# Kernel optimization log

Hardware: AMD Instinct MI355X
Metric: run time of the kernel (lower is better)

The kernel has to match this reference:

```python
import jax, jax.numpy as jnp
import numpy as np

N, E, IN_C, HID, OUT_C, HEADS, NUM_CLASSES = 50000, 800000, 128, 64, 64, 4, 40
NEG_SLOPE = 0.2


def _gat_conv(x, src, dst, W, a_src, a_dst, bias, heads, concat):
    # x: [N, F_in]; W: [F_in, heads*C]; a_src/a_dst: [1, heads, C]; bias: [out]
    n = x.shape[0]
    h = (x @ W).reshape(n, heads, -1)                      # [N, H, C]
    alpha_s = (h * a_src).sum(-1)                          # [N, H]
    alpha_d = (h * a_dst).sum(-1)                          # [N, H]
    e = jax.nn.leaky_relu(alpha_s[src] + alpha_d[dst], NEG_SLOPE)  # [E, H]
    # scatter-softmax over incoming edges of each dst node
    emax = jax.ops.segment_max(e, dst, num_segments=n)
    emax = jnp.where(jnp.isfinite(emax), emax, 0.0)
    ee = jnp.exp(e - emax[dst])
    denom = jax.ops.segment_sum(ee, dst, num_segments=n) + 1e-16
    w = ee / denom[dst]                                    # [E, H]
    out = jax.ops.segment_sum(h[src] * w[:, :, None], dst, num_segments=n)  # [N, H, C]
    out = out.reshape(n, -1) if concat else out.mean(axis=1)
    return out + bias


def setup_inputs() -> dict:
    key = jax.random.key(0)
    ks = jax.random.split(key, 12)
    s1 = 1.0 / np.sqrt(IN_C)
    s2 = 1.0 / np.sqrt(HID * HEADS)
    s3 = 1.0 / np.sqrt(OUT_C)
    return {
        "x": jax.random.normal(ks[0], (N, IN_C), dtype=jnp.float32),
        "edge_index": jax.random.randint(ks[1], (2, E), 0, N, dtype=jnp.int64),
        "W1": jax.random.normal(ks[2], (IN_C, HEADS * HID), dtype=jnp.float32) * s1,
        "att_src1": jax.random.normal(ks[3], (1, HEADS, HID), dtype=jnp.float32) * s1,
        "att_dst1": jax.random.normal(ks[4], (1, HEADS, HID), dtype=jnp.float32) * s1,
        "b1": jnp.zeros((HEADS * HID,), dtype=jnp.float32),
        "W2": jax.random.normal(ks[5], (HEADS * HID, OUT_C), dtype=jnp.float32) * s2,
        "att_src2": jax.random.normal(ks[6], (1, 1, OUT_C), dtype=jnp.float32) * s2,
        "att_dst2": jax.random.normal(ks[7], (1, 1, OUT_C), dtype=jnp.float32) * s2,
        "b2": jnp.zeros((OUT_C,), dtype=jnp.float32),
        "fc_w": jax.random.normal(ks[8], (OUT_C, NUM_CLASSES), dtype=jnp.float32) * s3,
        "fc_b": jnp.zeros((NUM_CLASSES,), dtype=jnp.float32),
    }


def reference(x, edge_index, W1, att_src1, att_dst1, b1, W2, att_src2, att_dst2, b2, fc_w, fc_b):
    n = x.shape[0]
    loops = jnp.arange(n, dtype=edge_index.dtype)
    ei = jnp.concatenate([edge_index, jnp.stack([loops, loops])], axis=1)  # add self-loops (PyG default)
    src, dst = ei[0], ei[1]
    h = jax.nn.relu(_gat_conv(x, src, dst, W1, att_src1, att_dst1, b1, HEADS, True))
    h = jax.nn.relu(_gat_conv(h, src, dst, W2, att_src2, att_dst2, b2, 1, False))
    # dropout p=0.01 is identity in eval mode
    pooled = h.mean(axis=0, keepdims=True)                 # global mean pool -> [1, OUT_C]
    logits = pooled @ fc_w + fc_b
    return jax.nn.log_softmax(logits, axis=1)
```

## Files before the change

kernel.cpp:

```cpp
#include <hip/hip_runtime.h>
#include <hip/hip_bf16.h>
#include <math.h>

#define NEG_SLOPE 0.2f
#define CHUNK2 2048
#define PGROUPS 32

typedef __attribute__((ext_vector_type(8))) short bf16x8;
typedef __attribute__((ext_vector_type(4))) float f32x4;
typedef __attribute__((ext_vector_type(2))) float f32x2_t;

__device__ __forceinline__ float lrelu(float a) { return a >= 0.f ? a : NEG_SLOPE * a; }
__device__ __forceinline__ unsigned short f2bu(float v) {
  unsigned u = __float_as_uint(v);
  u += 0x7fffu + ((u >> 16) & 1u);
  return (unsigned short)(u >> 16);
}
__device__ __forceinline__ unsigned char f2fp8(float v) {
  return (unsigned char)(__builtin_amdgcn_cvt_pk_fp8_f32(v, v, 0, false) & 0xFF);
}

__global__ __launch_bounds__(256) void prep_kernel(
    const float* __restrict__ W1, unsigned short* __restrict__ w1t,
    const float* __restrict__ W2, unsigned short* __restrict__ w2t,
    const int* __restrict__ ei, int* __restrict__ bhist,
    int E0, int Etot, int NBUCK, int wBlocks, int histBlocks) {
  __shared__ int hsm[256];
  int t = threadIdx.x;
  if (blockIdx.x < (unsigned)wBlocks) {
    const int tot1 = 128 * 256, tot2 = 256 * 64;
    for (int i = blockIdx.x * 256 + t; i < tot1 + tot2; i += wBlocks * 256) {
      if (i < tot1) { int k = i >> 8, n = i & 255; w1t[n * 128 + k] = f2bu(W1[i]); }
      else { int j = i - tot1; int k = j >> 6, n = j & 63; w2t[n * 256 + k] = f2bu(W2[j]); }
    }
  } else {
    int bid = blockIdx.x - wBlocks;
    hsm[t] = 0;
    __syncthreads();
    for (int e = bid * 256 + t; e < Etot; e += histBlocks * 256) {
      int dst = (e < E0) ? ei[E0 + e] : (e - E0);
      atomicAdd(&hsm[dst >> 8], 1);
    }
    __syncthreads();
    if (t < NBUCK && hsm[t]) atomicAdd(&bhist[t], hsm[t]);
  }
}

__global__ __launch_bounds__(256) void bucket_scan_kernel(const int* __restrict__ bhist,
    int* __restrict__ bucketOff, int* __restrict__ cursor, int* __restrict__ rowptrN,
    float* __restrict__ pooled_grp, int NBUCK, int Etot) {
  __shared__ int s[256];
  int t = threadIdx.x;
  int v = (t < NBUCK) ? bhist[t] : 0;
  s[t] = v;
  __syncthreads();
  for (int off = 1; off < 256; off <<= 1) {
    int u = (t >= off) ? s[t - off] : 0;
    __syncthreads();
    s[t] += u;
    __syncthreads();
  }
  int excl = s[t] - v;
  if (t < NBUCK) { bucketOff[t] = excl; cursor[t] = excl; }
  if (t == 0) { bucketOff[NBUCK] = Etot; *rowptrN = Etot; }
  for (int i = t; i < PGROUPS * 64; i += 256) pooled_grp[i] = 0.f;
}

__device__ void gemm1_tile(const float* __restrict__ x,
    const unsigned short* __restrict__ BT, unsigned char* __restrict__ C8,
    const float* __restrict__ att_s, const float* __restrict__ att_d,
    float* __restrict__ as_, float* __restrict__ ad_,
    int M, int bx, int by, char* smem) {
  const int K = 128;
  unsigned short (*Al)[40] = (unsigned short (*)[40])smem;
  unsigned short (*Bt)[40] = (unsigned short (*)[40])(smem + 5120);
  float* sal = (float*)(smem + 10240);
  float* sad = (float*)(smem + 10752);
  const int tid = threadIdx.x;
  const int row0 = by * 64, col0 = bx * 64;
  const int lane = tid & 63, wave = tid >> 6;
  const int wm = wave >> 1, wn = wave & 1;
  const int l15 = lane & 15, q = lane >> 4;

  f32x4 acc[2][2] = {};

  const int rr = tid >> 2, rc = (tid & 3) * 8;

  for (int k0 = 0; k0 < K; k0 += 32) {
    float4 v0 = make_float4(0.f, 0.f, 0.f, 0.f), v1 = v0;
    if (row0 + rr < M) {
      const float* ap = x + (size_t)(row0 + rr) * K + k0 + rc;
      v0 = *(const float4*)ap;
      v1 = *(const float4*)(ap + 4);
    }
    *(ushort4*)&Al[rr][rc] = make_ushort4(f2bu(v0.x), f2bu(v0.y), f2bu(v0.z), f2bu(v0.w));
    *(ushort4*)&Al[rr][rc + 4] = make_ushort4(f2bu(v1.x), f2bu(v1.y), f2bu(v1.z), f2bu(v1.w));
    {
      const ushort4* bp = (const ushort4*)(BT + (size_t)(col0 + rr) * K + k0 + rc);
      *(ushort4*)&Bt[rr][rc] = bp[0];
      *(ushort4*)&Bt[rr][rc + 4] = bp[1];
    }
    __syncthreads();
    bf16x8 af[2], bf[2];
#pragma unroll
    for (int mi = 0; mi < 2; mi++)
      af[mi] = *(const bf16x8*)&Al[wm * 32 + mi * 16 + l15][q * 8];
#pragma unroll
    for (int ni = 0; ni < 2; ni++)
      bf[ni] = *(const bf16x8*)&Bt[wn * 32 + ni * 16 + l15][q * 8];
#pragma unroll
    for (int mi = 0; mi < 2; mi++)
#pragma unroll
      for (int ni = 0; ni < 2; ni++)
        acc[mi][ni] = __builtin_amdgcn_mfma_f32_16x16x32_bf16(af[mi], bf[ni], acc[mi][ni], 0, 0, 0);
    __syncthreads();
  }
#pragma unroll
  for (int mi = 0; mi < 2; mi++) {
#pragma unroll
    for (int r = 0; r < 4; r++) {
      int grow = row0 + wm * 32 + mi * 16 + q * 4 + r;
      if (grow < M) {
#pragma unroll
        for (int ni = 0; ni < 2; ni++) {
          int gcol = col0 + wn * 32 + ni * 16 + l15;
          C8[(size_t)grow * 256 + gcol] = f2fp8(acc[mi][ni][r]);
        }
      }
    }
  }
  float atts0 = att_s[col0 + wn * 32 + l15];
  float atts1 = att_s[col0 + wn * 32 + 16 + l15];
  float attd0 = att_d[col0 + wn * 32 + l15];
  float attd1 = att_d[col0 + wn * 32 + 16 + l15];
#pragma unroll
  for (int mi = 0; mi < 2; mi++) {
#pragma unroll
    for (int r = 0; r < 4; r++) {
      float vs = acc[mi][0][r] * atts0 + acc[mi][1][r] * atts1;
      float vd = acc[mi][0][r] * attd0 + acc[mi][1][r] * attd1;
#pragma unroll
      for (int off = 1; off < 16; off <<= 1) {
        vs += __shfl_xor(vs, off);
        vd += __shfl_xor(vd, off);
      }
      if (l15 == 0) {
        int rl = wm * 32 + mi * 16 + q * 4 + r;
        sal[wn * 64 + rl] = vs;
        sad[wn * 64 + rl] = vd;
      }
    }
  }
  __syncthreads();
  if (tid < 64) {
    int grow = row0 + tid;
    if (grow < M) {
      as_[(size_t)grow * 4 + bx] = sal[tid] + sal[64 + tid];
      ad_[(size_t)grow * 4 + bx] = sad[tid] + sad[64 + tid];
    }
  }
}

__global__ __launch_bounds__(256) void gemm1_scatter_kernel(
    const float* __restrict__ x, const unsigned short* __restrict__ BT,
    unsigned char* __restrict__ C8, const float* __restrict__ att_s,
    const float* __restrict__ att_d, float* __restrict__ as_, float* __restrict__ ad_,
    int M, const int* __restrict__ ei, int* __restrict__ cursor, int* __restrict__ pairs,
    int E0, int Etot, int NBUCK, int NSC) {
  __shared__ __align__(16) char smem[18432];
  if (blockIdx.x < (unsigned)NSC) {
    int2* stage = (int2*)smem;
    int* h = (int*)(smem + 16384);
    int* base = (int*)(smem + 17408);
    int t = threadIdx.x;
    int e0 = blockIdx.x * CHUNK2;
    h[t] = 0;
    __syncthreads();
    int cnt = Etot - e0;
    if (cnt > CHUNK2) cnt = CHUNK2;
    for (int i = t; i < cnt; i += 256) {
      int e = e0 + i;
      int s, d;
      if (e < E0) { s = ei[e]; d = ei[E0 + e]; } else { s = d = e - E0; }
      stage[i] = make_int2((s << 8) | (d & 255), d >> 8);
      atomicAdd(&h[d >> 8], 1);
    }
    __syncthreads();
    if (t < NBUCK && h[t]) base[t] = atomicAdd(&cursor[t], h[t]);
    __syncthreads();
    for (int i = t; i < cnt; i += 256) {
      int2 p = stage[i];
      int pos = atomicAdd(&base[p.y], 1);
      pairs[pos] = p.x;
    }
  } else {
    int flat = blockIdx.x - NSC;
    gemm1_tile(x, BT, C8, att_s, att_d, as_, ad_, M, flat % 4, flat / 4, smem);
  }
}

__global__ __launch_bounds__(256) void csr_build_kernel(const int* __restrict__ pairs,
    const int* __restrict__ bucketOff, int* __restrict__ rowptr, int* __restrict__ csr_src,
    int N) {
  int b = blockIdx.x, t = threadIdx.x;
  int base = bucketOff[b], cnt = bucketOff[b + 1] - base;
  int n0 = b << 8;
  __shared__ int h[256];
  __shared__ int s[256];
  __shared__ int ex[256];
  h[t] = 0;
  __syncthreads();
  for (int i = t; i < cnt; i += 256) atomicAdd(&h[pairs[base + i] & 255], 1);
  __syncthreads();
  int v = h[t];
  s[t] = v;
  __syncthreads();
  for (int off = 1; off < 256; off <<= 1) {
    int u = (t >= off) ? s[t - off] : 0;
    __syncthreads();
    s[t] += u;
    __syncthreads();
  }
  ex[t] = s[t] - v;
  if (n0 + t < N) rowptr[n0 + t] = base + ex[t];
  __syncthreads();
  for (int i = t; i < cnt; i += 256) {
    int p = pairs[base + i];
    int pos = atomicAdd(&ex[p & 255], 1);
    csr_src[base + pos] = ((unsigned)p) >> 8;
  }
}

#define ACCV(W, X) do {                                                        \
    f32x2_t w2_; w2_.x = (W); w2_.y = (W);                                     \
    av[0] += w2_ * __builtin_amdgcn_cvt_pk_f32_fp8((X).x, false);              \
    av[1] += w2_ * __builtin_amdgcn_cvt_pk_f32_fp8((X).x, true);               \
    av[2] += w2_ * __builtin_amdgcn_cvt_pk_f32_fp8((X).y, false);              \
    av[3] += w2_ * __builtin_amdgcn_cvt_pk_f32_fp8((X).y, true);               \
    av[4] += w2_ * __builtin_amdgcn_cvt_pk_f32_fp8((X).z, false);              \
    av[5] += w2_ * __builtin_amdgcn_cvt_pk_f32_fp8((X).z, true);               \
    av[6] += w2_ * __builtin_amdgcn_cvt_pk_f32_fp8((X).w, false);              \
    av[7] += w2_ * __builtin_amdgcn_cvt_pk_f32_fp8((X).w, true);               \
  } while (0)

__global__ __launch_bounds__(256) void aggr1_kernel(const int* __restrict__ rowptr,
    const int* __restrict__ csr_src, const float* __restrict__ as_,
    const float* __restrict__ ad_, const uint4* __restrict__ h1f8,
    const float* __restrict__ b1, unsigned short* __restrict__ out1, int Nn) {
  int lane = threadIdx.x & 63, wv = threadIdx.x >> 6;
  int q = lane >> 4, l15 = lane & 15;
  int n = (blockIdx.x * 4 + wv) * 4 + q;
  if (n >= Nn) return;
  int row = rowptr[n], deg = rowptr[n + 1] - row;
  int rowEnd = row + deg;
  int hh = l15 >> 2;
  float adv = ad_[n * 4 + hh];
  const uint4* hb = h1f8 + l15;
  f32x2_t av[8] = {};
  float wsum = 0.f;
  int p0 = row + l15;
  int idxv = (p0 < rowEnd) ? csr_src[p0] : 0;
  for (int s0 = 0; s0 < deg; s0 += 16) {
    int pn = row + s0 + 16 + l15;
    int idxn = (pn < rowEnd) ? csr_src[pn] : 0;
    int m = deg - s0;
    if (m > 16) m = 16;
    int j = 0;
    for (; j + 4 <= m; j += 4) {
      int i0 = __shfl(idxv, j, 16);
      int i1 = __shfl(idxv, j + 1, 16);
      int i2 = __shfl(idxv, j + 2, 16);
      int i3 = __shfl(idxv, j + 3, 16);
      float a0v = as_[i0 * 4 + hh];
      float a1v = as_[i1 * 4 + hh];
      float a2v = as_[i2 * 4 + hh];
      float a3v = as_[i3 * 4 + hh];
      uint4 x0 = hb[(size_t)i0 * 16];
      uint4 x1 = hb[(size_t)i1 * 16];
      uint4 x2 = hb[(size_t)i2 * 16];
      uint4 x3 = hb[(size_t)i3 * 16];
      float w0 = __expf(lrelu(a0v + adv));
      float w1 = __expf(lrelu(a1v + adv));
      float w2 = __expf(lrelu(a2v + adv));
      float w3 = __expf(lrelu(a3v + adv));
      wsum += (w0 + w1) + (w2 + w3);
      ACCV(w0, x0);
      ACCV(w1, x1);
      ACCV(w2, x2);
      ACCV(w3, x3);
    }
    for (; j < m; j++) {
      int i0 = __shfl(idxv, j, 16);
      float a0v = as_[i0 * 4 + hh];
      uint4 x0 = hb[(size_t)i0 * 16];
      float w0 = __expf(lrelu(a0v + adv));
      wsum += w0;
      ACCV(w0, x0);
    }
    idxv = idxn;
  }
  float vinv = 1.f / wsum;
  int c0i = l15 * 16;
  unsigned short ob[16];
#pragma unroll
  for (int k = 0; k < 4; k++) {
    float4 bb = *(const float4*)(b1 + c0i + k * 4);
    float r0 = fmaf(av[k * 2].x, vinv, bb.x);
    float r1 = fmaf(av[k * 2].y, vinv, bb.y);
    float r2 = fmaf(av[k * 2 + 1].x, vinv, bb.z);
    float r3 = fmaf(av[k * 2 + 1].y, vinv, bb.w);
    ob[k * 4 + 0] = f2bu(r0 > 0.f ? r0 : 0.f);
    ob[k * 4 + 1] = f2bu(r1 > 0.f ? r1 : 0.f);
    ob[k * 4 + 2] = f2bu(r2 > 0.f ? r2 : 0.f);
    ob[k * 4 + 3] = f2bu(r3 > 0.f ? r3 : 0.f);
  }
  *(ushort4*)(out1 + (size_t)n * 256 + c0i) = *(ushort4*)&ob[0];
  *(ushort4*)(out1 + (size_t)n * 256 + c0i + 4) = *(ushort4*)&ob[4];
  *(ushort4*)(out1 + (size_t)n * 256 + c0i + 8) = *(ushort4*)&ob[8];
  *(ushort4*)(out1 + (size_t)n * 256 + c0i + 12) = *(ushort4*)&ob[12];
}

__global__ __launch_bounds__(256) void gemm2_kernel(const unsigned short* __restrict__ A,
    const unsigned short* __restrict__ BT, unsigned char* __restrict__ C8,
    const float* __restrict__ att_s, const float* __restrict__ att_d,
    float* __restrict__ as_, float* __restrict__ ad_, int M) {
  const int K = 256, Ncol = 64;
  __shared__ __align__(16) char smem[11264];
  unsigned short (*Al)[40] = (unsigned short (*)[40])smem;
  unsigned short (*Bt)[40] = (unsigned short (*)[40])(smem + 5120);
  float* sal = (float*)(smem + 10240);
  float* sad = (float*)(smem + 10752);
  const int tid = threadIdx.x;
  const int row0 = blockIdx.x * 64;
  const int lane = tid & 63, wave = tid >> 6;
  const int wm = wave >> 1, wn = wave & 1;
  const int l15 = lane & 15, q = lane >> 4;

  f32x4 acc[2][2] = {};
  const int rr = tid >> 2, rc = (tid & 3) * 8;

  for (int k0 = 0; k0 < K; k0 += 32) {
    ushort4 av0 = make_ushort4(0, 0, 0, 0), av1 = av0;
    if (row0 + rr < M) {
      const ushort4* ap = (const ushort4*)(A + (size_t)(row0 + rr) * K + k0 + rc);
      av0 = ap[0]; av1 = ap[1];
    }
    *(ushort4*)&Al[rr][rc] = av0;
    *(ushort4*)&Al[rr][rc + 4] = av1;
    {
      const ushort4* bp = (const ushort4*)(BT + (size_t)rr * K + k0 + rc);
      *(ushort4*)&Bt[rr][rc] = bp[0];
      *(ushort4*)&Bt[rr][rc + 4] = bp[1];
    }
    __syncthreads();
    bf16x8 af[2], bf[2];
#pragma unroll
    for (int mi = 0; mi < 2; mi++)
      af[mi] = *(const bf16x8*)&Al[wm * 32 + mi * 16 + l15][q * 8];
#pragma unroll
    for (int ni = 0; ni < 2; ni++)
      bf[ni] = *(const bf16x8*)&Bt[wn * 32 + ni * 16 + l15][q * 8];
#pragma unroll
    for (int mi = 0; mi < 2; mi++)
#pragma unroll
      for (int ni = 0; ni < 2; ni++)
        acc[mi][ni] = __builtin_amdgcn_mfma_f32_16x16x32_bf16(af[mi], bf[ni], acc[mi][ni], 0, 0, 0);
    __syncthreads();
  }
#pragma unroll
  for (int mi = 0; mi < 2; mi++) {
#pragma unroll
    for (int r = 0; r < 4; r++) {
      int grow = row0 + wm * 32 + mi * 16 + q * 4 + r;
      if (grow < M) {
#pragma unroll
        for (int ni = 0; ni < 2; ni++) {
          int gcol = wn * 32 + ni * 16 + l15;
          C8[(size_t)grow * Ncol + gcol] = f2fp8(acc[mi][ni][r]);
        }
      }
    }
  }
  float atts0 = att_s[wn * 32 + l15], atts1 = att_s[wn * 32 + 16 + l15];
  float attd0 = att_d[wn * 32 + l15], attd1 = att_d[wn * 32 + 16 + l15];
#pragma unroll
  for (int mi = 0; mi < 2; mi++) {
#pragma unroll
    for (int r = 0; r < 4; r++) {
      float vs = acc[mi][0][r] * atts0 + acc[mi][1][r] * atts1;
      float vd = acc[mi][0][r] * attd0 + acc[mi][1][r] * attd1;
#pragma unroll
      for (int off = 1; off < 16; off <<= 1) {
        vs += __shfl_xor(vs, off);
        vd += __shfl_xor(vd, off);
      }
      if (l15 == 0) {
        int rl = wm * 32 + mi * 16 + q * 4 + r;
        sal[wn * 64 + rl] = vs;
        sad[wn * 64 + rl] = vd;
      }
    }
  }
  __syncthreads();
  if (tid < 64) {
    int grow = row0 + tid;
    if (grow < M) {
      as_[grow] = sal[tid] + sal[64 + tid];
      ad_[grow] = sad[tid] + sad[64 + tid];
    }
  }
}

__global__ __launch_bounds__(256) void aggr2_pool_kernel(const int* __restrict__ rowptr,
    const int* __restrict__ csr_src, const float* __restrict__ as_,
    const float* __restrict__ ad_, const unsigned* __restrict__ h2f8,
    const float* __restrict__ b2, float* __restrict__ pooled_grp, int Nn) {
  int lane = threadIdx.x & 63, wv = threadIdx.x >> 6;
  int q = lane >> 4, l15 = lane & 15;
  int c0 = l15 * 4;
  const unsigned* hb = h2f8 + l15;
  f32x2_t pv0 = {0.f, 0.f}, pv1 = {0.f, 0.f};
  int stream = (blockIdx.x * 4 + wv) * 4 + q;
  int nstreams = gridDim.x * 16;
  for (int n = stream; n < Nn; n += nstreams) {
    int row = rowptr[n], deg = rowptr[n + 1] - row;
    int rowEnd = row + deg;
    float adv = ad_[n];
    f32x2_t a01 = {0.f, 0.f}, a23 = {0.f, 0.f};
    float wsum = 0.f;
    int pp = row + l15;
    int idxv = (pp < rowEnd) ? csr_src[pp] : 0;
    for (int s0 = 0; s0 < deg; s0 += 16) {
      int pn = row + s0 + 16 + l15;
      int idxn = (pn < rowEnd) ? csr_src[pn] : 0;
      int m = deg - s0;
      if (m > 16) m = 16;
      int j = 0;
      for (; j + 8 <= m; j += 8) {
        int id[8];
        float al[8];
        unsigned xv[8];
#pragma unroll
        for (int u = 0; u < 8; u++) id[u] = __shfl(idxv, j + u, 16);
#pragma unroll
        for (int u = 0; u < 8; u++) al[u] = as_[id[u]];
#pragma unroll
        for (int u = 0; u < 8; u++) xv[u] = hb[(size_t)id[u] * 16];
#pragma unroll
        for (int u = 0; u < 8; u++) {
          float w = __expf(lrelu(al[u] + adv));
          wsum += w;
          f32x2_t w2_; w2_.x = w; w2_.y = w;
          a01 += w2_ * __builtin_amdgcn_cvt_pk_f32_fp8(xv[u], false);
          a23 += w2_ * __builtin_amdgcn_cvt_pk_f32_fp8(xv[u], true);
        }
      }
      for (; j + 4 <= m; j += 4) {
        int id[4];
        float al[4];
        unsigned xv[4];
#pragma unroll
        for (int u = 0; u < 4; u++) id[u] = __shfl(idxv, j + u, 16);
#pragma unroll
        for (int u = 0; u < 4; u++) al[u] = as_[id[u]];
#pragma unroll
        for (int u = 0; u < 4; u++) xv[u] = hb[(size_t)id[u] * 16];
#pragma unroll
        for (int u = 0; u < 4; u++) {
          float w = __expf(lrelu(al[u] + adv));
          wsum += w;
          f32x2_t w2_; w2_.x = w; w2_.y = w;
          a01 += w2_ * __builtin_amdgcn_cvt_pk_f32_fp8(xv[u], false);
          a23 += w2_ * __builtin_amdgcn_cvt_pk_f32_fp8(xv[u], true);
        }
      }
      for (; j < m; j++) {
        int i0 = __shfl(idxv, j, 16);
        float w = __expf(lrelu(as_[i0] + adv));
        wsum += w;
        unsigned xvv = hb[(size_t)i0 * 16];
        f32x2_t w2_; w2_.x = w; w2_.y = w;
        a01 += w2_ * __builtin_amdgcn_cvt_pk_f32_fp8(xvv, false);
        a23 += w2_ * __builtin_amdgcn_cvt_pk_f32_fp8(xvv, true);
      }
      idxv = idxn;
    }
    float vinv = 1.f / wsum;
    float4 bb = *(const float4*)(b2 + c0);
    float r0 = fmaf(a01.x, vinv, bb.x), r1 = fmaf(a01.y, vinv, bb.y);
    float r2 = fmaf(a23.x, vinv, bb.z), r3 = fmaf(a23.y, vinv, bb.w);
    pv0.x += r0 > 0.f ? r0 : 0.f; pv0.y += r1 > 0.f ? r1 : 0.f;
    pv1.x += r2 > 0.f ? r2 : 0.f; pv1.y += r3 > 0.f ? r3 : 0.f;
  }
  __shared__ float4 sred[4][4][16];
  sred[wv][q][l15] = make_float4(pv0.x, pv0.y, pv1.x, pv1.y);
  __syncthreads();
  if (threadIdx.x < 64) {
    int slot = threadIdx.x >> 2, comp = threadIdx.x & 3;
    float acc = 0.f;
#pragma unroll
    for (int i = 0; i < 4; i++)
#pragma unroll
      for (int j = 0; j < 4; j++) {
        float4 v = sred[i][j][slot];
        acc += comp == 0 ? v.x : (comp == 1 ? v.y : (comp == 2 ? v.z : v.w));
      }
    atomicAdd(&pooled_grp[(blockIdx.x & (PGROUPS - 1)) * 64 + slot * 4 + comp], acc);
  }
}

__global__ __launch_bounds__(64) void pool_head_kernel(const float* __restrict__ pooled_grp,
    const float* __restrict__ fc_w, const float* __restrict__ fc_b,
    float* __restrict__ out, float invN) {
  int t = threadIdx.x;
  __shared__ float pl[64];
  __shared__ float lg[40];
  __shared__ float lse;
  float acc = 0.f;
#pragma unroll
  for (int g = 0; g < PGROUPS; g++) acc += pooled_grp[g * 64 + t];
  pl[t] = acc * invN;
  __syncthreads();
  if (t < 40) {
    float sm = fc_b[t];
    for (int c = 0; c < 64; c++) sm = fmaf(pl[c], fc_w[c * 40 + t], sm);
    lg[t] = sm;
  }
  __syncthreads();
  if (t == 0) {
    float m = -1e30f;
    for (int j = 0; j < 40; j++) m = fmaxf(m, lg[j]);
    float su = 0.f;
    for (int j = 0; j < 40; j++) su += expf(lg[j] - m);
    lse = m + logf(su);
  }
  __syncthreads();
  if (t < 40) out[t] = lg[t] - lse;
}

extern "C" void kernel_launch(void* const* d_in, const int* in_sizes, int n_in,
                              void* d_out, int out_size, void* d_ws, size_t ws_size,
                              hipStream_t stream) {
  const float* x        = (const float*)d_in[0];
  const int*   ei       = (const int*)d_in[1];
  const float* W1       = (const float*)d_in[2];
  const float* att_src1 = (const float*)d_in[3];
  const float* att_dst1 = (const float*)d_in[4];
  const float* b1       = (const float*)d_in[5];
  const float* W2       = (const float*)d_in[6];
  const float* att_src2 = (const float*)d_in[7];
  const float* att_dst2 = (const float*)d_in[8];
  const float* b2       = (const float*)d_in[9];
  const float* fc_w     = (const float*)d_in[10];
  const float* fc_b     = (const float*)d_in[11];
  float* out = (float*)d_out;

  const int N    = in_sizes[0] / 128;
  const int E0   = in_sizes[1] / 2;
  const int Etot = E0 + N;
  const int NBUCK = (N + 255) >> 8;
  const int NSC  = (Etot + CHUNK2 - 1) / CHUNK2;
  const int GBY  = (N + 63) / 64;
  const int AGG2_BLOCKS = 2048;

  char* wsb = (char*)d_ws;
  size_t o = 0;
  auto alloc = [&](size_t bytes) { char* p = wsb + o; o += (bytes + 15) & ~(size_t)15; return p; };
  unsigned short* w1t  = (unsigned short*)alloc(256 * 128 * 2);
  unsigned short* w2t  = (unsigned short*)alloc(64 * 256 * 2);
  unsigned char*  h1f8 = (unsigned char*)alloc((size_t)N * 256);
  unsigned char*  h2   = (unsigned char*)alloc((size_t)N * 64);
  unsigned short* out1 = (unsigned short*)alloc((size_t)N * 256 * 2);
  float* as1  = (float*)alloc((size_t)N * 4 * 4);
  float* ad1  = (float*)alloc((size_t)N * 4 * 4);
  float* as2  = (float*)alloc((size_t)N * 4);
  float* ad2  = (float*)alloc((size_t)N * 4);
  int* rowptr = (int*)alloc((size_t)(N + 1) * 4);
  int* bhist  = (int*)alloc(256 * 4);
  int* bucketOff = (int*)alloc(257 * 4);
  int* cursor = (int*)alloc(256 * 4);
  int* pairs  = (int*)alloc((size_t)Etot * 4);
  int* csr_src = (int*)alloc((size_t)Etot * 4);
  float* pooled_grp = (float*)alloc((size_t)PGROUPS * 64 * 4);

  dim3 blk(256);

  hipMemsetAsync(bhist, 0, 256 * sizeof(int), stream);
  prep_kernel<<<16 + 256, blk, 0, stream>>>(W1, w1t, W2, w2t, ei, bhist,
                                            E0, Etot, NBUCK, 16, 256);
  bucket_scan_kernel<<<1, blk, 0, stream>>>(bhist, bucketOff, cursor, rowptr + N,
                                            pooled_grp, NBUCK, Etot);

  gemm1_scatter_kernel<<<NSC + 4 * GBY, blk, 0, stream>>>(
      x, w1t, h1f8, att_src1, att_dst1, as1, ad1, N,
      ei, cursor, pairs, E0, Etot, NBUCK, NSC);
  csr_build_kernel<<<NBUCK, blk, 0, stream>>>(pairs, bucketOff, rowptr, csr_src, N);

  aggr1_kernel<<<(N + 15) / 16, blk, 0, stream>>>(rowptr, csr_src, as1, ad1,
                                                  (const uint4*)h1f8, b1, out1, N);

  gemm2_kernel<<<GBY, blk, 0, stream>>>(out1, w2t, h2, att_src2, att_dst2, as2, ad2, N);
  aggr2_pool_kernel<<<AGG2_BLOCKS, blk, 0, stream>>>(rowptr, csr_src, as2, ad2,
                                                     (const unsigned*)h2, b2, pooled_grp, N);

  pool_head_kernel<<<1, 64, 0, stream>>>(pooled_grp, fc_w, fc_b, out, 1.0f / (float)N);
}
```

Baseline: 226.2 us.

## Use full-width GEMM1 tiles and simplify edge-gather loops in aggregation kernels

GEMM1 now computes a 64x256 tile per block, with each wave owning one head's 64 columns. This removes the 4x column split, the re-reading and bf16 conversion of x per column block, and the shared-memory cross-wave reduction for the attention logits. Both aggregation kernels drop the shuffle-based, 16-wide prefetched index loop and instead load csr_src directly in clamped batches of 8, masking out the tail weights. The new tiles use more registers (16 accumulators) and a larger shared buffer, and the tail batches do redundant gathers that could hurt low-degree nodes.

```diff
diff --git a/kernel.cpp b/kernel.cpp
--- a/kernel.cpp
+++ b/kernel.cpp
@@ -70,93 +70,76 @@
     const unsigned short* __restrict__ BT, unsigned char* __restrict__ C8,
     const float* __restrict__ att_s, const float* __restrict__ att_d,
     float* __restrict__ as_, float* __restrict__ ad_,
-    int M, int bx, int by, char* smem) {
-  const int K = 128;
+    int M, int by, char* smem) {
   unsigned short (*Al)[40] = (unsigned short (*)[40])smem;
   unsigned short (*Bt)[40] = (unsigned short (*)[40])(smem + 5120);
-  float* sal = (float*)(smem + 10240);
-  float* sad = (float*)(smem + 10752);
   const int tid = threadIdx.x;
-  const int row0 = by * 64, col0 = bx * 64;
+  const int row0 = by * 64;
   const int lane = tid & 63, wave = tid >> 6;
-  const int wm = wave >> 1, wn = wave & 1;
   const int l15 = lane & 15, q = lane >> 4;
 
-  f32x4 acc[2][2] = {};
-
+  f32x4 acc[4][4] = {};
   const int rr = tid >> 2, rc = (tid & 3) * 8;
 
-  for (int k0 = 0; k0 < K; k0 += 32) {
+  for (int k0 = 0; k0 < 128; k0 += 32) {
     float4 v0 = make_float4(0.f, 0.f, 0.f, 0.f), v1 = v0;
     if (row0 + rr < M) {
-      const float* ap = x + (size_t)(row0 + rr) * K + k0 + rc;
+      const float* ap = x + (size_t)(row0 + rr) * 128 + k0 + rc;
       v0 = *(const float4*)ap;
       v1 = *(const float4*)(ap + 4);
     }
     *(ushort4*)&Al[rr][rc] = make_ushort4(f2bu(v0.x), f2bu(v0.y), f2bu(v0.z), f2bu(v0.w));
     *(ushort4*)&Al[rr][rc + 4] = make_ushort4(f2bu(v1.x), f2bu(v1.y), f2bu(v1.z), f2bu(v1.w));
     {
-      const ushort4* bp = (const ushort4*)(BT + (size_t)(col0 + rr) * K + k0 + rc);
-      *(ushort4*)&Bt[rr][rc] = bp[0];
-      *(ushort4*)&Bt[rr][rc + 4] = bp[1];
-    }
-    __syncthreads();
-    bf16x8 af[2], bf[2];
-#pragma unroll
-    for (int mi = 0; mi < 2; mi++)
-      af[mi] = *(const bf16x8*)&Al[wm * 32 + mi * 16 + l15][q * 8];
-#pragma unroll
-    for (int ni = 0; ni < 2; ni++)
-      bf[ni] = *(const bf16x8*)&Bt[wn * 32 + ni * 16 + l15][q * 8];
-#pragma unroll
-    for (int mi = 0; mi < 2; mi++)
-#pragma unroll
-      for (int ni = 0; ni < 2; ni++)
+      const ushort4* bp = (const ushort4*)(BT + (size_t)tid * 128 + k0);
+#pragma unroll
+      for (int i = 0; i < 8; i++) *(ushort4*)&Bt[tid][i * 4] = bp[i];
+    }
+    __syncthreads();
+    bf16x8 af[4], bf[4];
+#pragma unroll
+    for (int mi = 0; mi < 4; mi++)
+      af[mi] = *(const bf16x8*)&Al[mi * 16 + l15][q * 8];
+#pragma unroll
+    for (int ni = 0; ni < 4; ni++)
+      bf[ni] = *(const bf16x8*)&Bt[wave * 64 + ni * 16 + l15][q * 8];
+#pragma unroll
+    for (int mi = 0; mi < 4; mi++)
+#pragma unroll
+      for (int ni = 0; ni < 4; ni++)
         acc[mi][ni] = __builtin_amdgcn_mfma_f32_16x16x32_bf16(af[mi], bf[ni], acc[mi][ni], 0, 0, 0);
     __syncthreads();
   }
-#pragma unroll
-  for (int mi = 0; mi < 2; mi++) {
+  float atts[4], attd[4];
+#pragma unroll
+  for (int ni = 0; ni < 4; ni++) {
+    atts[ni] = att_s[wave * 64 + ni * 16 + l15];
+    attd[ni] = att_d[wave * 64 + ni * 16 + l15];
+  }
+#pragma unroll
+  for (int mi = 0; mi < 4; mi++) {
 #pragma unroll
     for (int r = 0; r < 4; r++) {
-      int grow = row0 + wm * 32 + mi * 16 + q * 4 + r;
-      if (grow < M) {
-#pragma unroll
-        for (int ni = 0; ni < 2; ni++) {
-          int gcol = col0 + wn * 32 + ni * 16 + l15;
-          C8[(size_t)grow * 256 + gcol] = f2fp8(acc[mi][ni][r]);
-        }
-      }
-    }
-  }
-  float atts0 = att_s[col0 + wn * 32 + l15];
-  float atts1 = att_s[col0 + wn * 32 + 16 + l15];
-  float attd0 = att_d[col0 + wn * 32 + l15];
-  float attd1 = att_d[col0 + wn * 32 + 16 + l15];
-#pragma unroll
-  for (int mi = 0; mi < 2; mi++) {
-#pragma unroll
-    for (int r = 0; r < 4; r++) {
-      float vs = acc[mi][0][r] * atts0 + acc[mi][1][r] * atts1;
-      float vd = acc[mi][0][r] * attd0 + acc[mi][1][r] * attd1;
+      int grow = row0 + mi * 16 + q * 4 + r;
+      bool ok = grow < M;
+      if (ok) {
+#pragma unroll
+        for (int ni = 0; ni < 4; ni++)
+          C8[(size_t)grow * 256 + wave * 64 + ni * 16 + l15] = f2fp8(acc[mi][ni][r]);
+      }
+      float vs = acc[mi][0][r] * atts[0] + acc[mi][1][r] * atts[1]
+               + acc[mi][2][r] * atts[2] + acc[mi][3][r] * atts[3];
+      float vd = acc[mi][0][r] * attd[0] + acc[mi][1][r] * attd[1]
+               + acc[mi][2][r] * attd[2] + acc[mi][3][r] * attd[3];
 #pragma unroll
       for (int off = 1; off < 16; off <<= 1) {
         vs += __shfl_xor(vs, off);
         vd += __shfl_xor(vd, off);
       }
-      if (l15 == 0) {
-        int rl = wm * 32 + mi * 16 + q * 4 + r;
-        sal[wn * 64 + rl] = vs;
-        sad[wn * 64 + rl] = vd;
-      }
-    }
-  }
-  __syncthreads();
-  if (tid < 64) {
-    int grow = row0 + tid;
-    if (grow < M) {
-      as_[(size_t)grow * 4 + bx] = sal[tid] + sal[64 + tid];
-      ad_[(size_t)grow * 4 + bx] = sad[tid] + sad[64 + tid];
+      if (ok && l15 == 0) {
+        as_[(size_t)grow * 4 + wave] = vs;
+        ad_[(size_t)grow * 4 + wave] = vd;
+      }
     }
   }
 }
@@ -167,7 +150,7 @@
     const float* __restrict__ att_d, float* __restrict__ as_, float* __restrict__ ad_,
     int M, const int* __restrict__ ei, int* __restrict__ cursor, int* __restrict__ pairs,
     int E0, int Etot, int NBUCK, int NSC) {
-  __shared__ __align__(16) char smem[18432];
+  __shared__ __align__(16) char smem[25600];
   if (blockIdx.x < (unsigned)NSC) {
     int2* stage = (int2*)smem;
     int* h = (int*)(smem + 16384);
@@ -194,8 +177,7 @@
       pairs[pos] = p.x;
     }
   } else {
-    int flat = blockIdx.x - NSC;
-    gemm1_tile(x, BT, C8, att_s, att_d, as_, ad_, M, flat % 4, flat / 4, smem);
+    gemm1_tile(x, BT, C8, att_s, att_d, as_, ad_, M, blockIdx.x - NSC, smem);
   }
 }
 
@@ -252,52 +234,31 @@
   int n = (blockIdx.x * 4 + wv) * 4 + q;
   if (n >= Nn) return;
   int row = rowptr[n], deg = rowptr[n + 1] - row;
-  int rowEnd = row + deg;
   int hh = l15 >> 2;
   float adv = ad_[n * 4 + hh];
   const uint4* hb = h1f8 + l15;
   f32x2_t av[8] = {};
   float wsum = 0.f;
-  int p0 = row + l15;
-  int idxv = (p0 < rowEnd) ? csr_src[p0] : 0;
-  for (int s0 = 0; s0 < deg; s0 += 16) {
-    int pn = row + s0 + 16 + l15;
-    int idxn = (pn < rowEnd) ? csr_src[pn] : 0;
-    int m = deg - s0;
-    if (m > 16) m = 16;
-    int j = 0;
-    for (; j + 4 <= m; j += 4) {
-      int i0 = __shfl(idxv, j, 16);
-      int i1 = __shfl(idxv, j + 1, 16);
-      int i2 = __shfl(idxv, j + 2, 16);
-      int i3 = __shfl(idxv, j + 3, 16);
-      float a0v = as_[i0 * 4 + hh];
-      float a1v = as_[i1 * 4 + hh];
-      float a2v = as_[i2 * 4 + hh];
-      float a3v = as_[i3 * 4 + hh];
-      uint4 x0 = hb[(size_t)i0 * 16];
-      uint4 x1 = hb[(size_t)i1 * 16];
-      uint4 x2 = hb[(size_t)i2 * 16];
-      uint4 x3 = hb[(size_t)i3 * 16];
-      float w0 = __expf(lrelu(a0v + adv));
-      float w1 = __expf(lrelu(a1v + adv));
-      float w2 = __expf(lrelu(a2v + adv));
-      float w3 = __expf(lrelu(a3v + adv));
-      wsum += (w0 + w1) + (w2 + w3);
-      ACCV(w0, x0);
-      ACCV(w1, x1);
-      ACCV(w2, x2);
-      ACCV(w3, x3);
-    }
-    for (; j < m; j++) {
-      int i0 = __shfl(idxv, j, 16);
-      float a0v = as_[i0 * 4 + hh];
-      uint4 x0 = hb[(size_t)i0 * 16];
-      float w0 = __expf(lrelu(a0v + adv));
-      wsum += w0;
-      ACCV(w0, x0);
-    }
-    idxv = idxn;
+  for (int s = 0; s < deg; s += 8) {
+    int id[8];
+    float al[8];
+    uint4 xv[8];
+#pragma unroll
+    for (int u = 0; u < 8; u++) {
+      int p = s + u;
+      if (p > deg - 1) p = deg - 1;
+      id[u] = csr_src[row + p];
+    }
+#pragma unroll
+    for (int u = 0; u < 8; u++) al[u] = as_[id[u] * 4 + hh];
+#pragma unroll
+    for (int u = 0; u < 8; u++) xv[u] = hb[(size_t)id[u] * 16];
+#pragma unroll
+    for (int u = 0; u < 8; u++) {
+      float w = (s + u < deg) ? __expf(lrelu(al[u] + adv)) : 0.f;
+      wsum += w;
+      ACCV(w, xv[u]);
+    }
   }
   float vinv = 1.f / wsum;
   int c0i = l15 * 16;
@@ -424,66 +385,31 @@
   int nstreams = gridDim.x * 16;
   for (int n = stream; n < Nn; n += nstreams) {
     int row = rowptr[n], deg = rowptr[n + 1] - row;
-    int rowEnd = row + deg;
     float adv = ad_[n];
     f32x2_t a01 = {0.f, 0.f}, a23 = {0.f, 0.f};
     float wsum = 0.f;
-    int pp = row + l15;
-    int idxv = (pp < rowEnd) ? csr_src[pp] : 0;
-    for (int s0 = 0; s0 < deg; s0 += 16) {
-      int pn = row + s0 + 16 + l15;
-      int idxn = (pn < rowEnd) ? csr_src[pn] : 0;
-      int m = deg - s0;
-      if (m > 16) m = 16;
-      int j = 0;
-      for (; j + 8 <= m; j += 8) {
-        int id[8];
-        float al[8];
-        unsigned xv[8];
-#pragma unroll
-        for (int u = 0; u < 8; u++) id[u] = __shfl(idxv, j + u, 16);
-#pragma unroll
-        for (int u = 0; u < 8; u++) al[u] = as_[id[u]];
-#pragma unroll
-        for (int u = 0; u < 8; u++) xv[u] = hb[(size_t)id[u] * 16];
-#pragma unroll
-        for (int u = 0; u < 8; u++) {
-          float w = __expf(lrelu(al[u] + adv));
-          wsum += w;
-          f32x2_t w2_; w2_.x = w; w2_.y = w;
-          a01 += w2_ * __builtin_amdgcn_cvt_pk_f32_fp8(xv[u], false);
-          a23 += w2_ * __builtin_amdgcn_cvt_pk_f32_fp8(xv[u], true);
-        }
-      }
-      for (; j + 4 <= m; j += 4) {
-        int id[4];
-        float al[4];
-        unsigned xv[4];
-#pragma unroll
-        for (int u = 0; u < 4; u++) id[u] = __shfl(idxv, j + u, 16);
-#pragma unroll
-        for (int u = 0; u < 4; u++) al[u] = as_[id[u]];
-#pragma unroll
-        for (int u = 0; u < 4; u++) xv[u] = hb[(size_t)id[u] * 16];
-#pragma unroll
-        for (int u = 0; u < 4; u++) {
-          float w = __expf(lrelu(al[u] + adv));
-          wsum += w;
-          f32x2_t w2_; w2_.x = w; w2_.y = w;
-          a01 += w2_ * __builtin_amdgcn_cvt_pk_f32_fp8(xv[u], false);
-          a23 += w2_ * __builtin_amdgcn_cvt_pk_f32_fp8(xv[u], true);
-        }
-      }
-      for (; j < m; j++) {
-        int i0 = __shfl(idxv, j, 16);
-        float w = __expf(lrelu(as_[i0] + adv));
+    for (int s = 0; s < deg; s += 8) {
+      int id[8];
+      float al[8];
+      unsigned xv[8];
+#pragma unroll
+      for (int u = 0; u < 8; u++) {
+        int p = s + u;
+        if (p > deg - 1) p = deg - 1;
+        id[u] = csr_src[row + p];
+      }
+#pragma unroll
+      for (int u = 0; u < 8; u++) al[u] = as_[id[u]];
+#pragma unroll
+      for (int u = 0; u < 8; u++) xv[u] = hb[(size_t)id[u] * 16];
+#pragma unroll
+      for (int u = 0; u < 8; u++) {
+        float w = (s + u < deg) ? __expf(lrelu(al[u] + adv)) : 0.f;
         wsum += w;
-        unsigned xvv = hb[(size_t)i0 * 16];
         f32x2_t w2_; w2_.x = w; w2_.y = w;
-        a01 += w2_ * __builtin_amdgcn_cvt_pk_f32_fp8(xvv, false);
-        a23 += w2_ * __builtin_amdgcn_cvt_pk_f32_fp8(xvv, true);
-      }
-      idxv = idxn;
+        a01 += w2_ * __builtin_amdgcn_cvt_pk_f32_fp8(xv[u], false);
+        a23 += w2_ * __builtin_amdgcn_cvt_pk_f32_fp8(xv[u], true);
+      }
     }
     float vinv = 1.f / wsum;
     float4 bb = *(const float4*)(b2 + c0);
@@ -591,7 +517,7 @@
   bucket_scan_kernel<<<1, blk, 0, stream>>>(bhist, bucketOff, cursor, rowptr + N,
                                             pooled_grp, NBUCK, Etot);
 
-  gemm1_scatter_kernel<<<NSC + 4 * GBY, blk, 0, stream>>>(
+  gemm1_scatter_kernel<<<NSC + GBY, blk, 0, stream>>>(
       x, w1t, h1f8, att_src1, att_dst1, as1, ad1, N,
       ei, cursor, pairs, E0, Etot, NBUCK, NSC);
   csr_build_kernel<<<NBUCK, blk, 0, stream>>>(pairs, bucketOff, rowptr, csr_src, N);
```

Result: faster. 217.0 us (median of 2 runs) (-4.0%).
